# Performance work log

Hardware: AMD Instinct MI355X
Metric: run time of the kernel (lower is better)

## Reference

```python
import jax, jax.numpy as jnp
import numpy as np

NUM_HEADS = 16
LN_EPS = 1e-5


def pos_encoding(length, d):
    pos = jnp.arange(length, dtype=jnp.float32)[:, None]
    i = jnp.arange(d, dtype=jnp.float32)[None, :]
    angle = pos / jnp.power(10000.0, (2.0 * jnp.floor(i / 2.0)) / d)
    return jnp.where((jnp.arange(d) % 2) == 0, jnp.sin(angle), jnp.cos(angle))


def rel_shift(x):
    # x: (B, H, l, m) -> TXL shift trick
    b, h, l, m = x.shape
    x = jnp.concatenate([x, jnp.zeros((b, h, l, 1), x.dtype)], axis=-1)
    x = x.reshape(b, h, l * (m + 1))
    return x[:, :, l - 1:-1].reshape(b, h, l, m)


def layer_norm(x, g, b):
    mu = jnp.mean(x, axis=-1, keepdims=True)
    var = jnp.mean(jnp.square(x - mu), axis=-1, keepdims=True)
    return (x - mu) * jax.lax.rsqrt(var + LN_EPS) * g + b


def setup_inputs() -> dict:
    key = jax.random.key(0)
    B, S, M, D, L, V = 2, 1024, 1024, 1024, 4, 32000
    ks = jax.random.split(key, 32)
    s = 0.02
    d = {
        'inputs': jax.random.randint(ks[0], (B, S), 0, V, dtype=jnp.int32),
        'mems': jax.random.normal(ks[1], (L, B, M, D), jnp.float32),
        'emb': jax.random.normal(ks[2], (V, D), jnp.float32) * s,
        'Wq': jax.random.normal(ks[3], (L, D, D), jnp.float32) * s,
        'bq': jnp.zeros((L, D), jnp.float32),
        'Wke': jax.random.normal(ks[4], (L, D, D), jnp.float32) * s,
        'bke': jnp.zeros((L, D), jnp.float32),
        'Wkr': jax.random.normal(ks[5], (L, D, D), jnp.float32) * s,
        'bkr': jnp.zeros((L, D), jnp.float32),
        'Wv': jax.random.normal(ks[6], (L, D, D), jnp.float32) * s,
        'bv': jnp.zeros((L, D), jnp.float32),
        'Wo': jax.random.normal(ks[7], (L, D, D), jnp.float32) * s,
        'bo': jnp.zeros((L, D), jnp.float32),
        'ln1_g': jnp.ones((L, D), jnp.float32),
        'ln1_b': jnp.zeros((L, D), jnp.float32),
        'W1': jax.random.normal(ks[8], (L, D, D), jnp.float32) * s,
        'b1': jnp.zeros((L, D), jnp.float32),
        'W2': jax.random.normal(ks[9], (L, D, D), jnp.float32) * s,
        'b2': jnp.zeros((L, D), jnp.float32),
        'ln2_g': jnp.ones((L, D), jnp.float32),
        'ln2_b': jnp.zeros((L, D), jnp.float32),
        'Wh': jax.random.normal(ks[10], (D, D), jnp.float32) * s,
        'bh': jnp.zeros((D,), jnp.float32),
        'Wf': jax.random.normal(ks[11], (D, V), jnp.float32) * s,
        'bf': jnp.zeros((V,), jnp.float32),
        'next_mem_len': 1024,
    }
    return d


def reference(inputs, mems, emb, Wq, bq, Wke, bke, Wkr, bkr, Wv, bv, Wo, bo,
              ln1_g, ln1_b, W1, b1, W2, b2, ln2_g, ln2_b, Wh, bh, Wf, bf,
              next_mem_len):
    B, S = inputs.shape
    L, _, M, D = mems.shape
    T = M + S
    H = NUM_HEADS
    dh = D // H
    sqrt_dk = jnp.sqrt(jnp.float32(dh))

    rel_enc = pos_encoding(T, D)[::-1]  # (T, D), reversed
    # look-ahead mask: query i may attend key j iff j <= i + M
    mask = (jnp.arange(T)[None, :] > (jnp.arange(S)[:, None] + M)).astype(jnp.float32)
    mask = mask[None, None] * -1e9  # (1,1,S,T)

    x = emb[inputs] * jnp.sqrt(jnp.float32(D))  # (B,S,D)

    for l in range(L):
        x_tilde = jnp.concatenate([mems[l], x], axis=1)  # (B,T,D)
        q = (x @ Wq[l] + bq[l]).reshape(B, S, H, dh).transpose(0, 2, 1, 3)
        k = (x_tilde @ Wke[l] + bke[l]).reshape(B, T, H, dh).transpose(0, 2, 1, 3)
        v = (x_tilde @ Wv[l] + bv[l]).reshape(B, T, H, dh).transpose(0, 2, 1, 3)
        A = jnp.einsum('bhsd,bhtd->bhst', q, k)
        Qr = (rel_enc @ Wkr[l] + bkr[l]).reshape(T, H, dh).transpose(1, 0, 2)  # (H,T,dh)
        B_hat = jnp.einsum('bhsd,htd->bhst', q, Qr)
        score = (A + rel_shift(B_hat)) / sqrt_dk + mask
        attn = jax.nn.softmax(score, axis=-1)
        ctx = jnp.einsum('bhst,bhtd->bhsd', attn, v)
        ctx = ctx.transpose(0, 2, 1, 3).reshape(B, S, D)
        attn_out = ctx @ Wo[l] + bo[l]
        h1 = layer_norm(x + attn_out, ln1_g[l], ln1_b[l])
        ff = jax.nn.gelu(h1 @ W1[l] + b1[l], approximate=False) @ W2[l] + b2[l]
        x = layer_norm(h1 + ff, ln2_g[l], ln2_b[l])

    x = jax.nn.gelu(x @ Wh + bh, approximate=False)
    logits = x @ Wf + bf
    return logits
```

## Files before the change

### kernel.cpp

```cpp
#include <hip/hip_runtime.h>
#include <hip/hip_bf16.h>
#include <math.h>

typedef __attribute__((ext_vector_type(4))) float f32x4;
typedef __attribute__((ext_vector_type(8))) short s16x8;

#define BB 2
#define SS 1024
#define MEM 1024
#define DD 1024
#define LL 4
#define VV 32000
#define TT 2048
#define NH 16
#define DH 64

__device__ __forceinline__ short f2bf(float f) {
    unsigned u = __float_as_uint(f);
    u += 0x7fffu + ((u >> 16) & 1u);
    return (short)(u >> 16);
}

__device__ __forceinline__ float gelu_f(float x) {
    return 0.5f * x * (1.0f + erff(x * 0.70710678118654752f));
}

__device__ __forceinline__ void gll16(const short* g, short* l) {
    __builtin_amdgcn_global_load_lds(
        (__attribute__((address_space(1))) void*)(short*)g,
        (__attribute__((address_space(3))) void*)l, 16, 0, 0);
}

template<int WM, int WN>
__global__ __launch_bounds__(256) void gemm_bf16(
    const short* __restrict__ A, const short* __restrict__ Bt,
    const float* __restrict__ bias, const float* __restrict__ bias2,
    int nsplit, void* __restrict__ Cv, int N, int K, int nby, int act, int obf)
{
    constexpr int BM = WM * 32, BN = WN * 32;
    constexpr int NA = BM / 32, NB = BN / 32;
    __shared__ short a_s[BM * 64];
    __shared__ short b_s[BN * 64];
    const int tid  = threadIdx.x;
    const int lane = tid & 63;
    const int wave = tid >> 6;
    const int wr = wave >> 1, wc = wave & 1;
    const int fr = lane & 15, fg = lane >> 4;

    const int nwg = gridDim.x;
    const int bid = blockIdx.x;
    const int swz = ((nwg & 7) == 0) ? ((bid & 7) * (nwg >> 3) + (bid >> 3)) : bid;
    const size_t m0 = (size_t)(swz % nby) * BM;
    const size_t n0 = (size_t)(swz / nby) * BN;

    const short* gA[NA]; short* lA[NA];
    const short* gB[NB]; short* lB[NB];
    #pragma unroll
    for (int i = 0; i < NA; ++i) {
        const int s   = i * 256 + tid;
        const int row = (s >> 7) * 16 + (s & 15);
        const int kof = ((s >> 4) & 7) * 8;
        gA[i] = A + (m0 + row) * (size_t)K + kof;
        lA[i] = &a_s[s * 8];
    }
    #pragma unroll
    for (int i = 0; i < NB; ++i) {
        const int s   = i * 256 + tid;
        const int nn  = (s >> 7) * 16 + (s & 15);
        const int kof = ((s >> 4) & 7) * 8;
        gB[i] = Bt + (n0 + nn) * (size_t)K + kof;
        lB[i] = &b_s[s * 8];
    }

    f32x4 acc[WM][WN] = {};

    #pragma unroll
    for (int i = 0; i < NA; ++i) gll16(gA[i], lA[i]);
    #pragma unroll
    for (int i = 0; i < NB; ++i) gll16(gB[i], lB[i]);

    const int nt = K >> 6;
    for (int t = 0; t < nt; ++t) {
        __syncthreads();
        s16x8 af[WM][2], bf[WN][2];
        #pragma unroll
        for (int mi = 0; mi < WM; ++mi)
            #pragma unroll
            for (int h = 0; h < 2; ++h)
                af[mi][h] = *(const s16x8*)&a_s[((wr*WM + mi)*128 + (h*4 + fg)*16 + fr) * 8];
        #pragma unroll
        for (int ni = 0; ni < WN; ++ni)
            #pragma unroll
            for (int h = 0; h < 2; ++h)
                bf[ni][h] = *(const s16x8*)&b_s[((wc*WN + ni)*128 + (h*4 + fg)*16 + fr) * 8];
        if (t + 1 < nt) {
            __syncthreads();
            const int koff = (t + 1) << 6;
            #pragma unroll
            for (int i = 0; i < NA; ++i) gll16(gA[i] + koff, lA[i]);
            #pragma unroll
            for (int i = 0; i < NB; ++i) gll16(gB[i] + koff, lB[i]);
        }
        #pragma unroll
        for (int mi = 0; mi < WM; ++mi)
            #pragma unroll
            for (int ni = 0; ni < WN; ++ni) {
                acc[mi][ni] = __builtin_amdgcn_mfma_f32_16x16x32_bf16(
                    af[mi][0], bf[ni][0], acc[mi][ni], 0, 0, 0);
                acc[mi][ni] = __builtin_amdgcn_mfma_f32_16x16x32_bf16(
                    af[mi][1], bf[ni][1], acc[mi][ni], 0, 0, 0);
            }
    }

    float* Cf = (float*)Cv;
    short* Cb = (short*)Cv;
    #pragma unroll
    for (int mi = 0; mi < WM; ++mi) {
        #pragma unroll
        for (int ni = 0; ni < WN; ++ni) {
            const size_t r0 = m0 + wr*WM*16 + mi*16 + fg*4;
            const size_t c  = n0 + wc*WN*16 + ni*16 + fr;
            const float bb = (c < (size_t)nsplit) ? bias[c] : bias2[c - nsplit];
            #pragma unroll
            for (int rg = 0; rg < 4; ++rg) {
                float vv = acc[mi][ni][rg] + bb;
                if (act) vv = gelu_f(vv);
                if (obf) Cb[(r0 + rg)*(size_t)N + c] = f2bf(vv);
                else     Cf[(r0 + rg)*(size_t)N + c] = vv;
            }
        }
    }
}

#define READ_A8(MH, BUF) \
  _Pragma("unroll") for (int mf = 0; mf < 4; ++mf) \
  _Pragma("unroll") for (int kh = 0; kh < 2; ++kh) \
    aA[mf][kh] = *(const s16x8*)&lds[(BUF)*16384 + WR*8192 + (((MH)*4+mf)*128 + (kh*4+fg)*16 + fr)*8];

#define READ_B8(BUF) \
  _Pragma("unroll") for (int nf = 0; nf < 4; ++nf) \
  _Pragma("unroll") for (int kh = 0; kh < 2; ++kh) \
    bB[nf][kh] = *(const s16x8*)&lds[32768 + (BUF)*16384 + BH*8192 + ((BC4+nf)*128 + (kh*4+fg)*16 + fr)*8];

#define QUAD8(MH, NHX) \
  _Pragma("unroll") for (int mf = 0; mf < 4; ++mf) \
  _Pragma("unroll") for (int n2 = 0; n2 < 2; ++n2) { \
    acc[(MH)*4+mf][(NHX)*2+n2] = __builtin_amdgcn_mfma_f32_16x16x32_bf16( \
        aA[mf][0], bB[(NHX)*2+n2][0], acc[(MH)*4+mf][(NHX)*2+n2], 0, 0, 0); \
    acc[(MH)*4+mf][(NHX)*2+n2] = __builtin_amdgcn_mfma_f32_16x16x32_bf16( \
        aA[mf][1], bB[(NHX)*2+n2][1], acc[(MH)*4+mf][(NHX)*2+n2], 0, 0, 0); }

#define STAGE_A8(HH, BUF, KT) { \
    const short* g = pA0 + (HH)*(128*1024) + (KT)*64; \
    short* l = &lds[(BUF)*16384 + (HH)*8192 + tid*8]; \
    gll16(g, l); gll16(g + 64*1024, l + 512*8); }

#define STAGE_B8(HH, BUF, KT) { \
    const short* g = pB0 + (HH)*(128*1024) + (KT)*64; \
    short* l = &lds[32768 + (BUF)*16384 + (HH)*8192 + tid*8]; \
    gll16(g, l); gll16(g + 64*1024, l + 512*8); }

#define PHASE8(BUF, MH, NHX, RA, RB, SMAT, SH, SBUF, SKT, VMW) { \
    if (RA) { READ_A8(MH, BUF) } \
    if (RB) { READ_B8(BUF) } \
    if ((SMAT) == 0) STAGE_A8(SH, SBUF, SKT) else STAGE_B8(SH, SBUF, SKT) \
    __builtin_amdgcn_s_barrier(); \
    asm volatile("s_waitcnt lgkmcnt(0)" ::: "memory"); \
    __builtin_amdgcn_sched_barrier(0); \
    __builtin_amdgcn_s_setprio(1); \
    QUAD8(MH, NHX) \
    __builtin_amdgcn_s_setprio(0); \
    if (VMW) { asm volatile("s_waitcnt vmcnt(4)" ::: "memory"); } \
    __builtin_amdgcn_s_barrier(); }

__global__ __launch_bounds__(512, 2) void gemm8p(
    const short* __restrict__ A, const short* __restrict__ Bt,
    const float* __restrict__ bias, float* __restrict__ C, int N)
{
    extern __shared__ short lds[];
    const int tid  = threadIdx.x;
    const int lane = tid & 63;
    const int wave = tid >> 6;
    const int WR = wave >> 2;
    const int WC = wave & 3;
    const int BH = WC >> 1;
    const int BC4 = (WC & 1) * 4;
    const int fr = lane & 15, fg = lane >> 4;

    const int nwg = gridDim.x;
    const int bid = blockIdx.x;
    const int swz = ((nwg & 7) == 0) ? ((bid & 7) * (nwg >> 3) + (bid >> 3)) : bid;
    const size_t m0 = (size_t)(swz % 8) * 256;
    const size_t n0 = (size_t)(swz / 8) * 256;

    const int arow0 = (tid >> 7) * 16 + (tid & 15);
    const int aks0  = ((tid >> 4) & 7) * 8;
    const short* pA0 = A  + (m0 + arow0) * 1024 + aks0;
    const short* pB0 = Bt + (n0 + arow0) * 1024 + aks0;

    f32x4 acc[8][4] = {};
    s16x8 aA[4][2], bB[4][2];

    STAGE_B8(0, 0, 0) STAGE_B8(1, 0, 0)
    STAGE_A8(0, 0, 0) STAGE_A8(1, 0, 0)
    STAGE_B8(0, 1, 1) STAGE_B8(1, 1, 1)
    asm volatile("s_waitcnt vmcnt(4)" ::: "memory");
    __builtin_amdgcn_s_barrier();

    for (int it = 0; it < 8; ++it) {
        const int k1 = 2*it + 1;
        int k2 = 2*it + 2; if (k2 > 15) k2 = 15;
        int k3 = 2*it + 3; if (k3 > 15) k3 = 15;
        PHASE8(0, 0, 0, 1, 1, 0, 0, 1, k1, 0)
        PHASE8(0, 0, 1, 0, 0, 0, 1, 1, k1, 0)
        PHASE8(0, 1, 0, 1, 0, 1, 0, 0, k2, 0)
        PHASE8(0, 1, 1, 0, 0, 1, 1, 0, k2, 1)
        PHASE8(1, 0, 0, 1, 1, 0, 0, 0, k2, 0)
        PHASE8(1, 0, 1, 0, 0, 0, 1, 0, k2, 0)
        PHASE8(1, 1, 0, 1, 0, 1, 0, 1, k3, 0)
        PHASE8(1, 1, 1, 0, 0, 1, 1, 1, k3, 1)
    }

    #pragma unroll
    for (int mf = 0; mf < 8; ++mf) {
        #pragma unroll
        for (int nf = 0; nf < 4; ++nf) {
            const size_t r0 = m0 + WR*128 + mf*16 + fg*4;
            const size_t c  = n0 + WC*64 + nf*16 + fr;
            const float bb = bias[c];
            #pragma unroll
            for (int rg = 0; rg < 4; ++rg)
                C[(r0 + rg) * (size_t)N + c] = acc[mf][nf][rg] + bb;
        }
    }
}

__global__ __launch_bounds__(512, 2) void gemm8n(
    const short* __restrict__ A, const short* __restrict__ Bt,
    const float* __restrict__ bA, const float* __restrict__ bBp,
    const float* __restrict__ bCp, int s1, int s2,
    short* __restrict__ Cb, int N, int K, int nby)
{
    extern __shared__ short lds[];
    const int tid  = threadIdx.x;
    const int lane = tid & 63;
    const int wave = tid >> 6;
    const int WR = wave >> 2;
    const int WC = wave & 3;
    const int fr = lane & 15, fg = lane >> 4;

    const int nwg = gridDim.x;
    const int bid = blockIdx.x;
    const int swz = ((nwg & 7) == 0) ? ((bid & 7) * (nwg >> 3) + (bid >> 3)) : bid;
    const size_t m0 = (size_t)(swz % nby) * 256;
    const size_t n0 = (size_t)(swz / nby) * 128;

    const int rA  = (tid >> 7) * 16 + (tid & 15);
    const int ks8 = ((tid >> 4) & 7) * 8;
    const short* pA = A  + (m0 + rA) * (size_t)K + ks8;
    const short* pB = Bt + (n0 + rA) * (size_t)K + ks8;

    auto stageA = [&](int kt, int h, int buf) {
        const short* g = pA + (size_t)(h * 128) * K + kt * 64;
        short* l = &lds[buf * 16384 + h * 8192 + tid * 8];
        gll16(g, l);
        gll16(g + (size_t)64 * K, l + 512 * 8);
    };
    auto stageB = [&](int kt, int buf) {
        const short* g = pB + kt * 64;
        short* l = &lds[49152 + buf * 8192 + tid * 8];
        gll16(g, l);
        gll16(g + (size_t)64 * K, l + 512 * 8);
    };

    f32x4 acc[8][2] = {};
    const int nt = K >> 6;

    stageB(0, 0); stageA(0, 0, 0); stageA(0, 1, 0);
    stageA(1, 0, 1); stageA(1, 1, 1); stageB(1, 1);

    for (int J = 0; J < nt / 2; ++J) {
        const int t0 = 2 * J, t1 = 2 * J + 1;
        const int b0 = t0 % 3, b1 = t1 % 3;
        const int b2 = (t0 + 2) % 3, b3 = (t1 + 2) % 3;
        int s2k = t0 + 2; if (s2k >= nt) s2k = nt - 1;
        int s3k = t1 + 2; if (s3k >= nt) s3k = nt - 1;

        #pragma unroll
        for (int ph = 0; ph < 2; ++ph) {
            const int bt = ph ? b1 : b0;
            asm volatile("s_waitcnt vmcnt(6)" ::: "memory");
            __builtin_amdgcn_s_barrier();
            __builtin_amdgcn_sched_barrier(0);
            if (ph == 0) { stageB(s2k, b2); stageA(s2k, 0, b2); stageA(s2k, 1, b2); }
            else         { stageA(s3k, 0, b3); stageA(s3k, 1, b3); stageB(s3k, b3); }
            s16x8 bB[2][2];
            #pragma unroll
            for (int nf = 0; nf < 2; ++nf)
                #pragma unroll
                for (int kh = 0; kh < 2; ++kh)
                    bB[nf][kh] = *(const s16x8*)&lds[49152 + bt*8192 +
                        ((WC*2 + nf)*128 + (kh*4 + fg)*16 + fr) * 8];
            #pragma unroll
            for (int MH = 0; MH < 2; ++MH) {
                s16x8 aF[4][2];
                #pragma unroll
                for (int mf = 0; mf < 4; ++mf)
                    #pragma unroll
                    for (int kh = 0; kh < 2; ++kh)
                        aF[mf][kh] = *(const s16x8*)&lds[bt*16384 + WR*8192 +
                            ((MH*4 + mf)*128 + (kh*4 + fg)*16 + fr) * 8];
                asm volatile("s_waitcnt lgkmcnt(0)" ::: "memory");
                __builtin_amdgcn_sched_barrier(0);
                __builtin_amdgcn_s_setprio(1);
                #pragma unroll
                for (int mf = 0; mf < 4; ++mf)
                    #pragma unroll
                    for (int nf = 0; nf < 2; ++nf) {
                        acc[MH*4+mf][nf] = __builtin_amdgcn_mfma_f32_16x16x32_bf16(
                            aF[mf][0], bB[nf][0], acc[MH*4+mf][nf], 0, 0, 0);
                        acc[MH*4+mf][nf] = __builtin_amdgcn_mfma_f32_16x16x32_bf16(
                            aF[mf][1], bB[nf][1], acc[MH*4+mf][nf], 0, 0, 0);
                    }
                __builtin_amdgcn_s_setprio(0);
            }
        }
    }

    #pragma unroll
    for (int mf = 0; mf < 8; ++mf) {
        #pragma unroll
        for (int nf = 0; nf < 2; ++nf) {
            const size_t r0 = m0 + WR*128 + mf*16 + fg*4;
            const size_t c  = n0 + WC*32 + nf*16 + fr;
            const float bb = (c < (size_t)s1) ? bA[c]
                            : (c < (size_t)s2) ? bBp[c - s1] : bCp[c - s2];
            #pragma unroll
            for (int rg = 0; rg < 4; ++rg)
                Cb[(r0 + rg) * (size_t)N + c] = f2bf(acc[mf][nf][rg] + bb);
        }
    }
}

__global__ __launch_bounds__(256) void transpose7_kernel(
    const float* w0, const float* w1, const float* w2, const float* w3,
    const float* w4, const float* w5, const float* w6, short* out)
{
    __shared__ float t[32][33];
    const int z = blockIdx.z;
    const float* W;
    switch (z) {
        case 0: W = w0; break; case 1: W = w1; break; case 2: W = w2; break;
        case 3: W = w3; break; case 4: W = w4; break; case 5: W = w5; break;
        default: W = w6; break;
    }
    short* O = out + (size_t)z * DD * DD;
    const int tid = threadIdx.x;
    const int k0 = blockIdx.y * 32, n0 = blockIdx.x * 32;
    const int r = tid >> 3, c4 = (tid & 7) * 4;
    float4 v = *(const float4*)&W[(size_t)(k0 + r) * DD + n0 + c4];
    t[r][c4+0] = v.x; t[r][c4+1] = v.y; t[r][c4+2] = v.z; t[r][c4+3] = v.w;
    __syncthreads();
    short4 o;
    o.x = f2bf(t[c4+0][r]); o.y = f2bf(t[c4+1][r]);
    o.z = f2bf(t[c4+2][r]); o.w = f2bf(t[c4+3][r]);
    *(short4*)&O[(size_t)(n0 + r) * DD + k0 + c4] = o;
}

__global__ __launch_bounds__(256) void transposeF_kernel(
    const float* __restrict__ W, short* __restrict__ O)
{
    __shared__ float t[32][33];
    const int tid = threadIdx.x;
    const int k0 = blockIdx.y * 32, n0 = blockIdx.x * 32;
    const int r = tid >> 3, c4 = (tid & 7) * 4;
    float4 v = *(const float4*)&W[(size_t)(k0 + r) * VV + n0 + c4];
    t[r][c4+0] = v.x; t[r][c4+1] = v.y; t[r][c4+2] = v.z; t[r][c4+3] = v.w;
    __syncthreads();
    short4 o;
    o.x = f2bf(t[c4+0][r]); o.y = f2bf(t[c4+1][r]);
    o.z = f2bf(t[c4+2][r]); o.w = f2bf(t[c4+3][r]);
    *(short4*)&O[(size_t)(n0 + r) * DD + k0 + c4] = o;
}

__global__ __launch_bounds__(256) void attn_kernel(
    const short* __restrict__ q, const short* __restrict__ k,
    const short* __restrict__ v, const short* __restrict__ Qr,
    short* __restrict__ ctx, int kstr, int qstr)
{
    __shared__ short k_s[64][72];
    __shared__ short vT_s[64][72];
    __shared__ short qr_s[128][72];
    __shared__ float a_t[64][67];
    __shared__ short p_s[64][72];

    const int tid  = threadIdx.x;
    const int id   = blockIdx.x;
    const int bh   = id & 31;
    const int qi   = ((id >> 5) + bh) & 15;
    const int q0   = qi * 64;
    const int b    = bh >> 4;
    const int h    = bh & 15;
    const int hoff = h * DH;

    const int lane = tid & 63;
    const int wave = tid >> 6;
    const int fr   = lane & 15;
    const int fg   = lane >> 4;
    const int tk = tid >> 2, ck = (tid & 3) * 16;
    const int rq = tid >> 1, dq = (tid & 1) * 32;
    const int jq = tid >> 2, dq3 = (tid & 3) * 16;
    const int sr  = tid >> 2;
    const int sc0 = (tid & 3) * 16;

    const short* qrow = q + ((size_t)(b * TT + q0 + 16 * wave + fr)) * kstr + hoff;
    s16x8 aq0 = *(const s16x8*)(qrow + fg * 8);
    s16x8 aq1 = *(const s16x8*)(qrow + 32 + fg * 8);

    float m_r = -1e30f, l_r = 0.0f;

    const int t_end = q0 + 64 + MEM;
    const int u0b   = SS - 1 - q0 - 63;

    s16x8 kf0, kf1, vf0, vf1, rf0, rf1, rf2, rf3, rg0, rg1;
    auto loadKV = [&](int t0) {
        const short* kp = k + ((size_t)(b * TT + t0 + tk)) * kstr + hoff + ck;
        const short* vp = v + ((size_t)(b * TT + t0 + tk)) * kstr + hoff + ck;
        kf0 = *(const s16x8*)kp;  kf1 = *(const s16x8*)(kp + 8);
        vf0 = *(const s16x8*)vp;  vf1 = *(const s16x8*)(vp + 8);
    };
    {
        int u = u0b + rq;
        u = u < 0 ? 0 : (u > TT - 1 ? TT - 1 : u);
        const short* rp = Qr + (size_t)u * qstr + hoff + dq;
        rf0 = *(const s16x8*)rp;        rf1 = *(const s16x8*)(rp + 8);
        rf2 = *(const s16x8*)(rp + 16); rf3 = *(const s16x8*)(rp + 24);
    }
    auto loadQRring = [&](int tn) {
        int u = tn + u0b + 64 + jq;
        u = u < 0 ? 0 : (u > TT - 1 ? TT - 1 : u);
        const short* rp = Qr + (size_t)u * qstr + hoff + dq3;
        rg0 = *(const s16x8*)rp;
        rg1 = *(const s16x8*)(rp + 8);
    };
    loadKV(0);

    f32x4 opv[4] = {};
    const int nlo = 3 - wave, nhi = 7 - wave;

    for (int t0 = 0; t0 < t_end; t0 += 64) {
        asm volatile("" ::: "memory");
        __builtin_amdgcn_s_barrier();
        __builtin_amdgcn_sched_barrier(0);
        {
            *(s16x8*)&k_s[tk][ck]     = kf0;
            *(s16x8*)&k_s[tk][ck + 8] = kf1;
            #pragma unroll
            for (int i = 0; i < 8; ++i) {
                const int d0 = ck + i, d1 = ck + 8 + i;
                vT_s[d0][tk ^ (((d0 >> 3) & 3) << 3)] = vf0[i];
                vT_s[d1][tk ^ (((d1 >> 3) & 3) << 3)] = vf1[i];
            }
            if (t0 == 0) {
                *(s16x8*)&qr_s[rq][dq]      = rf0;
                *(s16x8*)&qr_s[rq][dq + 8]  = rf1;
                *(s16x8*)&qr_s[rq][dq + 16] = rf2;
                *(s16x8*)&qr_s[rq][dq + 24] = rf3;
            } else {
                const int slot = (t0 + 64 + jq) & 127;
                *(s16x8*)&qr_s[slot][dq3]     = rg0;
                *(s16x8*)&qr_s[slot][dq3 + 8] = rg1;
            }
        }
        if (t0 + 64 < t_end) { loadKV(t0 + 64); loadQRring(t0 + 64); }
        asm volatile("s_waitcnt lgkmcnt(0)" ::: "memory");
        __builtin_amdgcn_s_barrier();
        __builtin_amdgcn_sched_barrier(0);

        {
            #pragma unroll
            for (int n = 0; n < 4; ++n) {
                s16x8 b0 = *(const s16x8*)&k_s[16*n + fr][fg * 8];
                s16x8 b1 = *(const s16x8*)&k_s[16*n + fr][32 + fg * 8];
                f32x4 ca = {0, 0, 0, 0};
                ca = __builtin_amdgcn_mfma_f32_16x16x32_bf16(aq0, b0, ca, 0, 0, 0);
                ca = __builtin_amdgcn_mfma_f32_16x16x32_bf16(aq1, b1, ca, 0, 0, 0);
                #pragma unroll
                for (int rg = 0; rg < 4; ++rg)
                    a_t[16*wave + 4*fg + rg][16*n + fr] = ca[rg];
            }
        }
        {
            #pragma unroll
            for (int n = 0; n < 8; ++n) {
                if (n < nlo || n > nhi) continue;
                const int pr = (t0 + 16*n + fr) & 127;
                s16x8 c0 = *(const s16x8*)&qr_s[pr][fg * 8];
                s16x8 c1 = *(const s16x8*)&qr_s[pr][32 + fg * 8];
                f32x4 cb = {0, 0, 0, 0};
                cb = __builtin_amdgcn_mfma_f32_16x16x32_bf16(aq0, c0, cb, 0, 0, 0);
                cb = __builtin_amdgcn_mfma_f32_16x16x32_bf16(aq1, c1, cb, 0, 0, 0);
                #pragma unroll
                for (int rg = 0; rg < 4; ++rg) {
                    const int r  = 16*wave + 4*fg + rg;
                    const int tl = 16*n + fr - 63 + r;
                    if ((unsigned)tl < 64u) a_t[r][tl] += cb[rg];
                }
            }
        }

        {
            const int sg = q0 + sr;
            float e[16];
            float mx = -1e30f;
            #pragma unroll
            for (int j = 0; j < 16; ++j) {
                const int c = sc0 + j;
                float x = a_t[sr][c] * 0.125f;
                x = (t0 + c > sg + MEM) ? -1e30f : x;
                e[j] = x;
                mx = fmaxf(mx, x);
            }
            mx = fmaxf(mx, __shfl_xor(mx, 1, 64));
            mx = fmaxf(mx, __shfl_xor(mx, 2, 64));
            const float mn  = fmaxf(m_r, mx);
            const float scl = __expf(m_r - mn);
            float sum = 0.0f;
            s16x8 p0, p1;
            #pragma unroll
            for (int j = 0; j < 16; ++j) {
                float ev = __expf(e[j] - mn);
                sum += ev;
                if (j < 8) p0[j] = f2bf(ev); else p1[j - 8] = f2bf(ev);
            }
            sum += __shfl_xor(sum, 1, 64);
            sum += __shfl_xor(sum, 2, 64);
            l_r = l_r * scl + sum;
            m_r = mn;
            *(s16x8*)&p_s[sr][sc0]     = p0;
            *(s16x8*)&p_s[sr][sc0 + 8] = p1;

            f32x4 scv;
            #pragma unroll
            for (int rg = 0; rg < 4; ++rg) scv[rg] = __shfl(scl, 16*fg + 4*rg, 64);
            #pragma unroll
            for (int n = 0; n < 4; ++n)
                #pragma unroll
                for (int rg = 0; rg < 4; ++rg) opv[n][rg] *= scv[rg];
            s16x8 ap0 = *(const s16x8*)&p_s[16*wave + fr][fg * 8];
            s16x8 ap1 = *(const s16x8*)&p_s[16*wave + fr][32 + fg * 8];
            #pragma unroll
            for (int n = 0; n < 4; ++n) {
                const int d  = 16*n + fr;
                const int xw = (d >> 3) & 3;
                s16x8 bv0 = *(const s16x8*)&vT_s[d][(fg ^ xw) * 8];
                s16x8 bv1 = *(const s16x8*)&vT_s[d][32 + (fg ^ xw) * 8];
                opv[n] = __builtin_amdgcn_mfma_f32_16x16x32_bf16(ap0, bv0, opv[n], 0, 0, 0);
                opv[n] = __builtin_amdgcn_mfma_f32_16x16x32_bf16(ap1, bv1, opv[n], 0, 0, 0);
            }
        }
    }

    {
        f32x4 lv;
        #pragma unroll
        for (int rg = 0; rg < 4; ++rg) lv[rg] = __shfl(l_r, 16*fg + 4*rg, 64);
        #pragma unroll
        for (int rg = 0; rg < 4; ++rg) {
            const int r = 16*wave + 4*fg + rg;
            const float inv = 1.0f / lv[rg];
            short* op = ctx + ((size_t)(b * SS + q0 + r)) * DD + hoff;
            #pragma unroll
            for (int n = 0; n < 4; ++n)
                op[16*n + fr] = f2bf(opv[n][rg] * inv);
        }
    }
}

__global__ __launch_bounds__(256) void addln_kernel(
    const float* __restrict__ a, const float* __restrict__ b,
    const float* __restrict__ g, const float* __restrict__ be,
    float* __restrict__ out32, short* __restrict__ outbf)
{
    __shared__ float red[8];
    const int row = blockIdx.x;
    const int tid = threadIdx.x;
    const size_t base = (size_t)row * DD;
    const int c = tid * 4;
    float4 xa = *(const float4*)(a + base + c);
    float4 xb = *(const float4*)(b + base + c);
    float x0 = xa.x + xb.x, x1 = xa.y + xb.y, x2 = xa.z + xb.z, x3 = xa.w + xb.w;
    float s  = x0 + x1 + x2 + x3;
    float sq = x0 * x0 + x1 * x1 + x2 * x2 + x3 * x3;
    #pragma unroll
    for (int o = 32; o > 0; o >>= 1) {
        s  += __shfl_down(s, o, 64);
        sq += __shfl_down(sq, o, 64);
    }
    const int wv = tid >> 6;
    if ((tid & 63) == 0) { red[wv * 2] = s; red[wv * 2 + 1] = sq; }
    __syncthreads();
    float ts = red[0] + red[2] + red[4] + red[6];
    float tq = red[1] + red[3] + red[5] + red[7];
    float mu  = ts * (1.0f / DD);
    float var = tq * (1.0f / DD) - mu * mu;
    float rs  = rsqrtf(var + 1e-5f);
    float4 gv = *(const float4*)(g + c);
    float4 bv = *(const float4*)(be + c);
    float4 o4;
    o4.x = (x0 - mu) * rs * gv.x + bv.x;
    o4.y = (x1 - mu) * rs * gv.y + bv.y;
    o4.z = (x2 - mu) * rs * gv.z + bv.z;
    o4.w = (x3 - mu) * rs * gv.w + bv.w;
    *(float4*)(out32 + base + c) = o4;
    short4 ob;
    ob.x = f2bf(o4.x); ob.y = f2bf(o4.y); ob.z = f2bf(o4.z); ob.w = f2bf(o4.w);
    *(short4*)(outbf + base + c) = ob;
}

__global__ __launch_bounds__(256) void embed_kernel(
    const int* __restrict__ inp, const float* __restrict__ emb,
    float* __restrict__ x32, short* __restrict__ xbf)
{
    const int row = blockIdx.x;
    const int c = threadIdx.x * 4;
    const int idx = inp[row];
    float4 vv = *(const float4*)(emb + (size_t)idx * DD + c);
    vv.x *= 32.0f; vv.y *= 32.0f; vv.z *= 32.0f; vv.w *= 32.0f;
    *(float4*)(x32 + (size_t)row * DD + c) = vv;
    short4 ob;
    ob.x = f2bf(vv.x); ob.y = f2bf(vv.y); ob.z = f2bf(vv.z); ob.w = f2bf(vv.w);
    *(short4*)(xbf + (size_t)row * DD + c) = ob;
}

__global__ __launch_bounds__(256) void concat_kernel(
    const float* __restrict__ mems_l, const short* __restrict__ xbf,
    short* __restrict__ xt)
{
    size_t i = ((size_t)blockIdx.x * 256 + threadIdx.x) * 8;
    size_t bt = i / DD;
    int d = (int)(i - bt * DD);
    int b = (int)(bt / TT);
    int t = (int)(bt - (size_t)b * TT);
    s16x8 o;
    if (t < MEM) {
        const float* mp = mems_l + ((size_t)(b * MEM + t)) * DD + d;
        float4 a0 = *(const float4*)mp;
        float4 a1 = *(const float4*)(mp + 4);
        o[0] = f2bf(a0.x); o[1] = f2bf(a0.y); o[2] = f2bf(a0.z); o[3] = f2bf(a0.w);
        o[4] = f2bf(a1.x); o[5] = f2bf(a1.y); o[6] = f2bf(a1.z); o[7] = f2bf(a1.w);
    } else {
        o = *(const s16x8*)(xbf + ((size_t)(b * SS + (t - MEM))) * DD + d);
    }
    *(s16x8*)(xt + i) = o;
}

__global__ __launch_bounds__(256) void relenc_kernel(short* __restrict__ re)
{
    const int u = blockIdx.x;
    const int p = TT - 1 - u;
    const int i0 = threadIdx.x * 4;
    short4 o;
    #pragma unroll
    for (int j = 0; j < 4; ++j) {
        int i = i0 + j;
        float ex   = (float)(2 * (i >> 1)) * (1.0f / DD);
        float invf = __expf(-ex * 9.210340371976184f);
        float ang  = (float)p * invf;
        float val  = (i & 1) ? cosf(ang) : sinf(ang);
        ((short*)&o)[j] = f2bf(val);
    }
    *(short4*)&re[(size_t)u * DD + i0] = o;
}

extern "C" void kernel_launch(void* const* d_in, const int* in_sizes, int n_in,
                              void* d_out, int out_size, void* d_ws, size_t ws_size,
                              hipStream_t stream)
{
    const int*   inp  = (const int*)d_in[0];
    const float* mems = (const float*)d_in[1];
    const float* emb  = (const float*)d_in[2];
    const float* Wq   = (const float*)d_in[3];
    const float* bq   = (const float*)d_in[4];
    const float* Wke  = (const float*)d_in[5];
    const float* bke  = (const float*)d_in[6];
    const float* Wkr  = (const float*)d_in[7];
    const float* bkr  = (const float*)d_in[8];
    const float* Wv   = (const float*)d_in[9];
    const float* bv   = (const float*)d_in[10];
    const float* Wo   = (const float*)d_in[11];
    const float* bo   = (const float*)d_in[12];
    const float* ln1g = (const float*)d_in[13];
    const float* ln1b = (const float*)d_in[14];
    const float* W1   = (const float*)d_in[15];
    const float* b1   = (const float*)d_in[16];
    const float* W2   = (const float*)d_in[17];
    const float* b2   = (const float*)d_in[18];
    const float* ln2g = (const float*)d_in[19];
    const float* ln2b = (const float*)d_in[20];
    const float* Wh   = (const float*)d_in[21];
    const float* bh   = (const float*)d_in[22];
    const float* Wf   = (const float*)d_in[23];
    const float* bfb  = (const float*)d_in[24];

    hipFuncSetAttribute((const void*)gemm8p,
                        hipFuncAttributeMaxDynamicSharedMemorySize, 131072);
    hipFuncSetAttribute((const void*)gemm8n,
                        hipFuncAttributeMaxDynamicSharedMemorySize, 147456);

    char* wsb = (char*)d_ws;
    size_t off = 0;
    auto alloc = [&](size_t bytes) { char* p = wsb + off; off += (bytes + 255) & ~(size_t)255; return p; };
    float* h132  = (float*)alloc((size_t)BB*SS*DD*4);
    float* ao32  = (float*)alloc((size_t)BB*SS*DD*4);
    float* ff232 = (float*)alloc((size_t)BB*SS*DD*4);
    short* xt    = (short*)alloc((size_t)BB*TT*DD*2);
    short* qkvb  = (short*)alloc((size_t)BB*TT*3*DD*2);
    short* ctxb  = (short*)alloc((size_t)BB*SS*DD*2);
    short* ff1   = (short*)alloc((size_t)BB*SS*DD*2);
    float* x32   = (float*)alloc((size_t)BB*SS*DD*4);
    short* x_bf  = (short*)alloc((size_t)BB*SS*DD*2);
    short* whout = (short*)alloc((size_t)BB*SS*DD*2);
    short* rel   = (short*)alloc((size_t)TT*DD*2);
    short* qr4   = (short*)alloc((size_t)TT*4*DD*2);
    short* wt6   = (short*)alloc((size_t)6*DD*DD*2);
    short* wkr4  = (short*)h132;
    short* wft   = (short*)h132;

    relenc_kernel<<<TT, 256, 0, stream>>>(rel);
    embed_kernel<<<BB * SS, 256, 0, stream>>>(inp, emb, x32, x_bf);

    const size_t WOFF = (size_t)DD * DD;

    transpose7_kernel<<<dim3(32, 32, 4), 256, 0, stream>>>(
        Wkr + 0*WOFF, Wkr + 1*WOFF, Wkr + 2*WOFF, Wkr + 3*WOFF, Wq, Wq, Wq, wkr4);
    gemm8n<<<dim3((TT/256) * (4*DD/128)), 512, 147456, stream>>>(
        rel, wkr4, bkr, bkr, bkr, 4*DD, 4*DD, qr4, 4*DD, DD, TT/256);

    const int gSm = (DD / 64) * ((BB * SS) / 64);

    for (int l = 0; l < LL; ++l) {
        const size_t wo  = (size_t)l * DD * DD;
        const size_t bo_ = (size_t)l * DD;
        transpose7_kernel<<<dim3(32, 32, 6), 256, 0, stream>>>(
            Wq + wo, Wke + wo, Wv + wo, Wo + wo, W1 + wo, W2 + wo, Wq, wt6);
        concat_kernel<<<(BB * TT * DD / 8) / 256, 256, 0, stream>>>(
            mems + (size_t)l * BB * MEM * DD, x_bf, xt);
        gemm8n<<<dim3((BB*TT/256) * (3*DD/128)), 512, 147456, stream>>>(
            xt, wt6, bq + bo_, bke + bo_, bv + bo_, DD, 2*DD, qkvb, 3*DD, DD, BB*TT/256);
        attn_kernel<<<dim3((SS / 64) * BB * NH), 256, 0, stream>>>(
            qkvb + (size_t)MEM * 3 * DD, qkvb + DD, qkvb + 2 * DD,
            qr4 + (size_t)l * DD, ctxb, 3 * DD, 4 * DD);
        gemm_bf16<2,2><<<dim3(gSm), 256, 0, stream>>>(
            ctxb, wt6 + 3*WOFF, bo + bo_, bo + bo_, DD, ao32, DD, DD, (BB*SS)/64, 0, 0);
        addln_kernel<<<BB * SS, 256, 0, stream>>>(x32, ao32, ln1g + bo_, ln1b + bo_, h132, x_bf);
        gemm_bf16<2,2><<<dim3(gSm), 256, 0, stream>>>(
            x_bf, wt6 + 4*WOFF, b1 + bo_, b1 + bo_, DD, ff1, DD, DD, (BB*SS)/64, 1, 1);
        gemm_bf16<2,2><<<dim3(gSm), 256, 0, stream>>>(
            ff1, wt6 + 5*WOFF, b2 + bo_, b2 + bo_, DD, ff232, DD, DD, (BB*SS)/64, 0, 0);
        addln_kernel<<<BB * SS, 256, 0, stream>>>(h132, ff232, ln2g + bo_, ln2b + bo_, x32, x_bf);
    }

    transpose7_kernel<<<dim3(32, 32, 1), 256, 0, stream>>>(
        Wh, Wh, Wh, Wh, Wh, Wh, Wh, wt6);
    transposeF_kernel<<<dim3(VV / 32, DD / 32), 256, 0, stream>>>(Wf, wft);
    gemm_bf16<2,2><<<dim3(gSm), 256, 0, stream>>>(
        x_bf, wt6, bh, bh, DD, whout, DD, DD, (BB*SS)/64, 1, 1);
    gemm8p<<<dim3((VV / 256) * ((BB * SS) / 256)), 512, 131072, stream>>>(
        whout, wft, bfb, (float*)d_out, VV);
}
```

Before: 1.267 ms.

## Use K=128 tiles in small GEMMs and alias attention P buffer with score tile

```diff
diff --git a/kernel.cpp b/kernel.cpp
--- a/kernel.cpp
+++ b/kernel.cpp
@@ -32,15 +32,15 @@
 }
 
 template<int WM, int WN>
-__global__ __launch_bounds__(256) void gemm_bf16(
+__global__ __launch_bounds__(256) void gemm_k128(
     const short* __restrict__ A, const short* __restrict__ Bt,
     const float* __restrict__ bias, const float* __restrict__ bias2,
     int nsplit, void* __restrict__ Cv, int N, int K, int nby, int act, int obf)
 {
     constexpr int BM = WM * 32, BN = WN * 32;
-    constexpr int NA = BM / 32, NB = BN / 32;
-    __shared__ short a_s[BM * 64];
-    __shared__ short b_s[BN * 64];
+    constexpr int NA = BM / 16, NB = BN / 16;
+    __shared__ short a_s[BM * 128];
+    __shared__ short b_s[BN * 128];
     const int tid  = threadIdx.x;
     const int lane = tid & 63;
     const int wave = tid >> 6;
@@ -57,19 +57,13 @@
     const short* gB[NB]; short* lB[NB];
     #pragma unroll
     for (int i = 0; i < NA; ++i) {
-        const int s   = i * 256 + tid;
-        const int row = (s >> 7) * 16 + (s & 15);
-        const int kof = ((s >> 4) & 7) * 8;
-        gA[i] = A + (m0 + row) * (size_t)K + kof;
-        lA[i] = &a_s[s * 8];
+        gA[i] = A + (m0 + i * 16 + (tid & 15)) * (size_t)K + (tid >> 4) * 8;
+        lA[i] = &a_s[(i * 256 + tid) * 8];
     }
     #pragma unroll
     for (int i = 0; i < NB; ++i) {
-        const int s   = i * 256 + tid;
-        const int nn  = (s >> 7) * 16 + (s & 15);
-        const int kof = ((s >> 4) & 7) * 8;
-        gB[i] = Bt + (n0 + nn) * (size_t)K + kof;
-        lB[i] = &b_s[s * 8];
+        gB[i] = Bt + (n0 + i * 16 + (tid & 15)) * (size_t)K + (tid >> 4) * 8;
+        lB[i] = &b_s[(i * 256 + tid) * 8];
     }
 
     f32x4 acc[WM][WN] = {};
@@ -79,23 +73,23 @@
     #pragma unroll
     for (int i = 0; i < NB; ++i) gll16(gB[i], lB[i]);
 
-    const int nt = K >> 6;
+    const int nt = K >> 7;
     for (int t = 0; t < nt; ++t) {
         __syncthreads();
-        s16x8 af[WM][2], bf[WN][2];
+        s16x8 af[WM][4], bf[WN][4];
         #pragma unroll
         for (int mi = 0; mi < WM; ++mi)
             #pragma unroll
-            for (int h = 0; h < 2; ++h)
-                af[mi][h] = *(const s16x8*)&a_s[((wr*WM + mi)*128 + (h*4 + fg)*16 + fr) * 8];
+            for (int h = 0; h < 4; ++h)
+                af[mi][h] = *(const s16x8*)&a_s[((wr*WM + mi)*256 + (4*h + fg)*16 + fr) * 8];
         #pragma unroll
         for (int ni = 0; ni < WN; ++ni)
             #pragma unroll
-            for (int h = 0; h < 2; ++h)
-                bf[ni][h] = *(const s16x8*)&b_s[((wc*WN + ni)*128 + (h*4 + fg)*16 + fr) * 8];
+            for (int h = 0; h < 4; ++h)
+                bf[ni][h] = *(const s16x8*)&b_s[((wc*WN + ni)*256 + (4*h + fg)*16 + fr) * 8];
         if (t + 1 < nt) {
             __syncthreads();
-            const int koff = (t + 1) << 6;
+            const int koff = (t + 1) << 7;
             #pragma unroll
             for (int i = 0; i < NA; ++i) gll16(gA[i] + koff, lA[i]);
             #pragma unroll
@@ -104,12 +98,11 @@
         #pragma unroll
         for (int mi = 0; mi < WM; ++mi)
             #pragma unroll
-            for (int ni = 0; ni < WN; ++ni) {
-                acc[mi][ni] = __builtin_amdgcn_mfma_f32_16x16x32_bf16(
-                    af[mi][0], bf[ni][0], acc[mi][ni], 0, 0, 0);
-                acc[mi][ni] = __builtin_amdgcn_mfma_f32_16x16x32_bf16(
-                    af[mi][1], bf[ni][1], acc[mi][ni], 0, 0, 0);
-            }
+            for (int ni = 0; ni < WN; ++ni)
+                #pragma unroll
+                for (int h = 0; h < 4; ++h)
+                    acc[mi][ni] = __builtin_amdgcn_mfma_f32_16x16x32_bf16(
+                        af[mi][h], bf[ni][h], acc[mi][ni], 0, 0, 0);
     }
 
     float* Cf = (float*)Cv;
@@ -391,8 +384,7 @@
     __shared__ short k_s[64][72];
     __shared__ short vT_s[64][72];
     __shared__ short qr_s[128][72];
-    __shared__ float a_t[64][67];
-    __shared__ short p_s[64][72];
+    __shared__ float a_t[64][68];
 
     const int tid  = threadIdx.x;
     const int id   = blockIdx.x;
@@ -478,6 +470,7 @@
         __builtin_amdgcn_sched_barrier(0);
 
         {
+            __builtin_amdgcn_s_setprio(1);
             #pragma unroll
             for (int n = 0; n < 4; ++n) {
                 s16x8 b0 = *(const s16x8*)&k_s[16*n + fr][fg * 8];
@@ -489,6 +482,7 @@
                 for (int rg = 0; rg < 4; ++rg)
                     a_t[16*wave + 4*fg + rg][16*n + fr] = ca[rg];
             }
+            __builtin_amdgcn_s_setprio(0);
         }
         {
             #pragma unroll
@@ -537,8 +531,11 @@
             sum += __shfl_xor(sum, 2, 64);
             l_r = l_r * scl + sum;
             m_r = mn;
-            *(s16x8*)&p_s[sr][sc0]     = p0;
-            *(s16x8*)&p_s[sr][sc0 + 8] = p1;
+            short* prow = (short*)&a_t[sr][0];
+            *(s16x8*)&prow[sc0]     = p0;
+            *(s16x8*)&prow[sc0 + 8] = p1;
+            asm volatile("s_waitcnt lgkmcnt(0)" ::: "memory");
+            __builtin_amdgcn_sched_barrier(0);
 
             f32x4 scv;
             #pragma unroll
@@ -547,8 +544,10 @@
             for (int n = 0; n < 4; ++n)
                 #pragma unroll
                 for (int rg = 0; rg < 4; ++rg) opv[n][rg] *= scv[rg];
-            s16x8 ap0 = *(const s16x8*)&p_s[16*wave + fr][fg * 8];
-            s16x8 ap1 = *(const s16x8*)&p_s[16*wave + fr][32 + fg * 8];
+            const short* pv = (const short*)&a_t[16*wave + fr][0];
+            s16x8 ap0 = *(const s16x8*)&pv[fg * 8];
+            s16x8 ap1 = *(const s16x8*)&pv[32 + fg * 8];
+            __builtin_amdgcn_s_setprio(1);
             #pragma unroll
             for (int n = 0; n < 4; ++n) {
                 const int d  = 16*n + fr;
@@ -558,6 +557,7 @@
                 opv[n] = __builtin_amdgcn_mfma_f32_16x16x32_bf16(ap0, bv0, opv[n], 0, 0, 0);
                 opv[n] = __builtin_amdgcn_mfma_f32_16x16x32_bf16(ap1, bv1, opv[n], 0, 0, 0);
             }
+            __builtin_amdgcn_s_setprio(0);
         }
     }
 
@@ -751,12 +751,12 @@
         attn_kernel<<<dim3((SS / 64) * BB * NH), 256, 0, stream>>>(
             qkvb + (size_t)MEM * 3 * DD, qkvb + DD, qkvb + 2 * DD,
             qr4 + (size_t)l * DD, ctxb, 3 * DD, 4 * DD);
-        gemm_bf16<2,2><<<dim3(gSm), 256, 0, stream>>>(
+        gemm_k128<2,2><<<dim3(gSm), 256, 0, stream>>>(
             ctxb, wt6 + 3*WOFF, bo + bo_, bo + bo_, DD, ao32, DD, DD, (BB*SS)/64, 0, 0);
         addln_kernel<<<BB * SS, 256, 0, stream>>>(x32, ao32, ln1g + bo_, ln1b + bo_, h132, x_bf);
-        gemm_bf16<2,2><<<dim3(gSm), 256, 0, stream>>>(
+        gemm_k128<2,2><<<dim3(gSm), 256, 0, stream>>>(
             x_bf, wt6 + 4*WOFF, b1 + bo_, b1 + bo_, DD, ff1, DD, DD, (BB*SS)/64, 1, 1);
-        gemm_bf16<2,2><<<dim3(gSm), 256, 0, stream>>>(
+        gemm_k128<2,2><<<dim3(gSm), 256, 0, stream>>>(
             ff1, wt6 + 5*WOFF, b2 + bo_, b2 + bo_, DD, ff232, DD, DD, (BB*SS)/64, 0, 0);
         addln_kernel<<<BB * SS, 256, 0, stream>>>(h132, ff232, ln2g + bo_, ln2b + bo_, x32, x_bf);
     }
@@ -764,7 +764,7 @@
     transpose7_kernel<<<dim3(32, 32, 1), 256, 0, stream>>>(
         Wh, Wh, Wh, Wh, Wh, Wh, Wh, wt6);
     transposeF_kernel<<<dim3(VV / 32, DD / 32), 256, 0, stream>>>(Wf, wft);
-    gemm_bf16<2,2><<<dim3(gSm), 256, 0, stream>>>(
+    gemm_k128<2,2><<<dim3(gSm), 256, 0, stream>>>(
         x_bf, wt6, bh, bh, DD, whout, DD, DD, (BB*SS)/64, 1, 1);
     gemm8p<<<dim3((VV / 256) * ((BB * SS) / 256)), 512, 131072, stream>>>(
         whout, wft, bfb, (float*)d_out, VV);
```

Result: no change. 1.263 ms (-0.3%).
